# Kernel tuning notes

Hardware: AMD Instinct MI355X
Metric: run time of the kernel (lower is better)

The kernel has to match this reference:

```python
import jax, jax.numpy as jnp
import numpy as np
import math

B, N, NDIM = 8, 8192, 2
WIDTH, HEADS, OUT_C, LATENT_D = 128, 4, 128, 128
N_POINT, N_SAMPLE, RADIUS, PATCH = 128, 8, 0.2, 8
MAX_DEG = 15
POS_DIM = NDIM * (1 + 2 * MAX_DEG)  # 62
SELF_LAYERS = 3


def setup_inputs() -> dict:
    ks = jax.random.split(jax.random.key(0), 16)
    f32 = jnp.float32
    def nrm(k, shape, s=0.02):
        return jax.random.normal(k, shape, dtype=f32) * s
    W = WIDTH
    inp = {
        'points': jax.random.uniform(ks[0], (B, N, NDIM), dtype=f32),
        'pe_w': nrm(ks[1], (POS_DIM, W)), 'pe_b': jnp.zeros((W,), f32),
        'conv1_w': nrm(ks[2], (W, W + NDIM, PATCH, 1)), 'conv1_b': jnp.zeros((W,), f32),
        'conv2_w': nrm(ks[3], (W, W, PATCH, 1)), 'conv2_b': jnp.zeros((W,), f32),
        'output_tokens': jax.random.normal(ks[4], (LATENT_D, W), dtype=f32),
        'ln_pre_s': jnp.ones((W,), f32), 'ln_pre_b': jnp.zeros((W,), f32),
        'c_ln1_s': jnp.ones((W,), f32), 'c_ln1_b': jnp.zeros((W,), f32),
        'c_ln2_s': jnp.ones((W,), f32), 'c_ln2_b': jnp.zeros((W,), f32),
        'c_q_w': nrm(ks[5], (W, W)), 'c_q_b': jnp.zeros((W,), f32),
        'c_kv_w': nrm(ks[6], (W, 2 * W)), 'c_kv_b': jnp.zeros((2 * W,), f32),
        'c_proj_w': nrm(ks[7], (W, W)), 'c_proj_b': jnp.zeros((W,), f32),
        'c_ln3_s': jnp.ones((W,), f32), 'c_ln3_b': jnp.zeros((W,), f32),
        'c_mlp1_w': nrm(ks[8], (W, 4 * W)), 'c_mlp1_b': jnp.zeros((4 * W,), f32),
        'c_mlp2_w': nrm(ks[9], (4 * W, W)), 'c_mlp2_b': jnp.zeros((W,), f32),
        's_ln1_s': jnp.ones((SELF_LAYERS, W), f32), 's_ln1_b': jnp.zeros((SELF_LAYERS, W), f32),
        's_qkv_w': nrm(ks[10], (SELF_LAYERS, W, 3 * W)), 's_qkv_b': jnp.zeros((SELF_LAYERS, 3 * W), f32),
        's_proj_w': nrm(ks[11], (SELF_LAYERS, W, W)), 's_proj_b': jnp.zeros((SELF_LAYERS, W), f32),
        's_ln2_s': jnp.ones((SELF_LAYERS, W), f32), 's_ln2_b': jnp.zeros((SELF_LAYERS, W), f32),
        's_mlp1_w': nrm(ks[12], (SELF_LAYERS, W, 4 * W)), 's_mlp1_b': jnp.zeros((SELF_LAYERS, 4 * W), f32),
        's_mlp2_w': nrm(ks[13], (SELF_LAYERS, 4 * W, W)), 's_mlp2_b': jnp.zeros((SELF_LAYERS, W), f32),
        'ln_post_s': jnp.ones((W,), f32), 'ln_post_b': jnp.zeros((W,), f32),
        'out_w': nrm(ks[14], (W, OUT_C)), 'out_b': jnp.zeros((OUT_C,), f32),
    }
    return inp


def _layer_norm(x, s, b):
    m = jnp.mean(x, -1, keepdims=True)
    v = jnp.mean(jnp.square(x - m), -1, keepdims=True)
    return (x - m) * jax.lax.rsqrt(v + 1e-5) * s + b


def _posenc_nerf(x):
    # point-e nerf posenc: concat([x, sin(xb), sin(xb + pi/2)])
    scales = 2.0 ** jnp.arange(MAX_DEG, dtype=jnp.float32)
    xb = (x[..., None, :] * scales[:, None]).reshape(*x.shape[:-1], -1)
    emb = jnp.sin(jnp.concatenate([xb, xb + 0.5 * jnp.pi], axis=-1))
    return jnp.concatenate([x, emb], axis=-1)  # [..., C*(1+2*MAX_DEG)]


def _mha(q, k, v):
    b, tq, w = q.shape
    dh = w // HEADS
    qh = q.reshape(b, tq, HEADS, dh)
    kh = k.reshape(b, -1, HEADS, dh)
    vh = v.reshape(b, -1, HEADS, dh)
    scores = jnp.einsum('bqhd,bkhd->bhqk', qh, kh) * (1.0 / math.sqrt(dh))
    attn = jax.nn.softmax(scores, axis=-1)
    return jnp.einsum('bhqk,bkhd->bqhd', attn, vh).reshape(b, tq, w)


def _circ_conv(x, w, b):
    # Conv2d kernel (PATCH,1), stride 1, circular padding (PATCH//2, 0)
    p = PATCH // 2
    xp = jnp.concatenate([x[:, :, -p:], x, x[:, :, :p]], axis=2)
    y = jax.lax.conv_general_dilated(xp, w, (1, 1), 'VALID',
                                     dimension_numbers=('NCHW', 'OIHW', 'NCHW'))
    return y + b[None, :, None, None]


def _forward(points, pe_w, pe_b, conv1_w, conv1_b, conv2_w, conv2_b, output_tokens,
             ln_pre_s, ln_pre_b, c_ln1_s, c_ln1_b, c_ln2_s, c_ln2_b, c_q_w, c_q_b,
             c_kv_w, c_kv_b, c_proj_w, c_proj_b, c_ln3_s, c_ln3_b, c_mlp1_w, c_mlp1_b,
             c_mlp2_w, c_mlp2_b, s_ln1_s, s_ln1_b, s_qkv_w, s_qkv_b, s_proj_w, s_proj_b,
             s_ln2_s, s_ln2_b, s_mlp1_w, s_mlp1_b, s_mlp2_w, s_mlp2_b, ln_post_s, ln_post_b,
             out_w, out_b):
    bsz, n, _ = points.shape
    dataset_emb = _posenc_nerf(points) @ pe_w + pe_b             # [B,N,W]
    # ---- PointSetEmbedding (fps_method='first' -> first n_point centers) ----
    new_xyz = points[:, :N_POINT]                                # [B,S,2]
    sqr = jnp.sum(jnp.square(new_xyz[:, :, None] - points[:, None]), -1)  # [B,S,N]
    base = jnp.broadcast_to(jnp.arange(n, dtype=jnp.int32), sqr.shape)
    idx = jnp.where(sqr > RADIUS ** 2, n, base)
    idx = jnp.sort(idx, axis=-1)[:, :, :N_SAMPLE]
    idx = jnp.where(idx == n, idx[:, :, :1], idx)                # [B,S,K] ball-query indices
    gather = jax.vmap(lambda a, i: a[i])
    grouped_xyz = gather(points, idx) - new_xyz[:, :, None]      # [B,S,K,2] relative coords
    grouped_pts = gather(dataset_emb, idx)                       # [B,S,K,W]
    feats = jnp.concatenate([grouped_xyz, grouped_pts], -1)      # [B,S,K,W+2]
    x = jnp.transpose(feats, (0, 3, 2, 1))                       # [B,C,K,S]
    x = jax.nn.silu(_circ_conv(x, conv1_w, conv1_b))
    x = jax.nn.silu(_circ_conv(x, conv2_w, conv2_b))
    data_tokens = jnp.transpose(x.mean(axis=2), (0, 2, 1))       # [B,S,W]
    # ---- Perceiver: cross-attn then self-attn ----
    lat = jnp.broadcast_to(output_tokens[None], (bsz, LATENT_D, WIDTH))
    h = _layer_norm(jnp.concatenate([data_tokens, lat], axis=1), ln_pre_s, ln_pre_b)
    q = _layer_norm(h, c_ln1_s, c_ln1_b) @ c_q_w + c_q_b
    kv = _layer_norm(dataset_emb, c_ln2_s, c_ln2_b) @ c_kv_w + c_kv_b
    k, v = jnp.split(kv, 2, axis=-1)
    h = h + (_mha(q, k, v) @ c_proj_w + c_proj_b)
    t = _layer_norm(h, c_ln3_s, c_ln3_b)
    h = h + (jax.nn.gelu(t @ c_mlp1_w + c_mlp1_b, approximate=False) @ c_mlp2_w + c_mlp2_b)
    for i in range(SELF_LAYERS):
        qkv = _layer_norm(h, s_ln1_s[i], s_ln1_b[i]) @ s_qkv_w[i] + s_qkv_b[i]
        q, k, v = jnp.split(qkv, 3, axis=-1)
        h = h + (_mha(q, k, v) @ s_proj_w[i] + s_proj_b[i])
        t = _layer_norm(h, s_ln2_s[i], s_ln2_b[i])
        h = h + (jax.nn.gelu(t @ s_mlp1_w[i] + s_mlp1_b[i], approximate=False) @ s_mlp2_w[i] + s_mlp2_b[i])
    h = h[:, -LATENT_D:]
    return jnp.tanh(_layer_norm(h, ln_post_s, ln_post_b) @ out_w + out_b)


def reference(points, pe_w, pe_b, conv1_w, conv1_b, conv2_w, conv2_b, output_tokens,
              ln_pre_s, ln_pre_b, c_ln1_s, c_ln1_b, c_ln2_s, c_ln2_b, c_q_w, c_q_b,
              c_kv_w, c_kv_b, c_proj_w, c_proj_b, c_ln3_s, c_ln3_b, c_mlp1_w, c_mlp1_b,
              c_mlp2_w, c_mlp2_b, s_ln1_s, s_ln1_b, s_qkv_w, s_qkv_b, s_proj_w, s_proj_b,
              s_ln2_s, s_ln2_b, s_mlp1_w, s_mlp1_b, s_mlp2_w, s_mlp2_b, ln_post_s, ln_post_b,
              out_w, out_b):
    return _forward(points, pe_w, pe_b, conv1_w, conv1_b, conv2_w, conv2_b, output_tokens,
                    ln_pre_s, ln_pre_b, c_ln1_s, c_ln1_b, c_ln2_s, c_ln2_b, c_q_w, c_q_b,
                    c_kv_w, c_kv_b, c_proj_w, c_proj_b, c_ln3_s, c_ln3_b, c_mlp1_w, c_mlp1_b,
                    c_mlp2_w, c_mlp2_b, s_ln1_s, s_ln1_b, s_qkv_w, s_qkv_b, s_proj_w, s_proj_b,
                    s_ln2_s, s_ln2_b, s_mlp1_w, s_mlp1_b, s_mlp2_w, s_mlp2_b, ln_post_s, ln_post_b,
                    out_w, out_b)
```

## Files before the change

kernel.cpp:

```cpp
#include <hip/hip_runtime.h>
#include <math.h>


namespace {

constexpr int NP = 8192;
constexpr int WD = 128;
constexpr int POSD = 62;
constexpr float R2C = 0.04f;
constexpr float QSCALE = 0.17677669529663687f;
constexpr float HALFPI = 1.5707963705062866f;

typedef __bf16 bf16x8 __attribute__((ext_vector_type(8)));
typedef float f32x4 __attribute__((ext_vector_type(4)));
union U16B { uint4 u; bf16x8 h; unsigned short s[8]; };

__device__ __forceinline__ float b2f(unsigned short u) {
  unsigned v = (unsigned)u << 16;
  return __builtin_bit_cast(float, v);
}

constexpr size_t AO_WQ     = 0;
constexpr size_t AO_WKV    = 16384;
constexpr size_t AO_WPROJC = 49152;
constexpr size_t AO_WMLP1C = 65536;
constexpr size_t AO_WMLP2C = 131072;
constexpr size_t AO_WQKVS  = 196608;
constexpr size_t AO_WPROJS = 344064;
constexpr size_t AO_WMLP1S = 393216;
constexpr size_t AO_WMLP2S = 589824;
constexpr size_t AO_WOUT   = 786432;
constexpr size_t AO_W1B    = 802816;
constexpr size_t AO_W2B    = 937984;
constexpr size_t AO_TOT    = 1069056;

__global__ __launch_bounds__(256) void k_posenc(
    const float* __restrict__ pts, const float* __restrict__ pew,
    const float* __restrict__ peb, unsigned short* __restrict__ embb) {
  __shared__ float posT[62][36];
  const int tid = threadIdx.x;
  const int base = blockIdx.x * 32;
  for (int i = tid; i < 32 * POSD; i += 256) {
    int p = i / POSD, j = i % POSD;
    const float* pp = pts + (size_t)(base + p) * 2;
    float v;
    if (j < 2) {
      v = pp[j];
    } else if (j < 32) {
      int t = j - 2;
      v = sinf(pp[t & 1] * (float)(1 << (t >> 1)));
    } else {
      int t = j - 32;
      v = sinf(pp[t & 1] * (float)(1 << (t >> 1)) + HALFPI);
    }
    posT[j][p] = v;
  }
  __syncthreads();
  const int c = tid & 127, pg = tid >> 7;
  float acc[16];
  const float bias = peb[c];
#pragma unroll
  for (int k = 0; k < 16; ++k) acc[k] = bias;
  for (int j = 0; j < POSD; ++j) {
    float w = pew[j * WD + c];
    const float4 p0 = *(const float4*)&posT[j][pg * 16];
    const float4 p1 = *(const float4*)&posT[j][pg * 16 + 4];
    const float4 p2 = *(const float4*)&posT[j][pg * 16 + 8];
    const float4 p3 = *(const float4*)&posT[j][pg * 16 + 12];
    acc[0] += p0.x * w;  acc[1] += p0.y * w;
    acc[2] += p0.z * w;  acc[3] += p0.w * w;
    acc[4] += p1.x * w;  acc[5] += p1.y * w;
    acc[6] += p1.z * w;  acc[7] += p1.w * w;
    acc[8] += p2.x * w;  acc[9] += p2.y * w;
    acc[10] += p2.z * w; acc[11] += p2.w * w;
    acc[12] += p3.x * w; acc[13] += p3.y * w;
    acc[14] += p3.z * w; acc[15] += p3.w * w;
  }
#pragma unroll
  for (int k = 0; k < 16; ++k) {
    __bf16 bv = (__bf16)acc[k];
    embb[(size_t)(base + pg * 16 + k) * WD + c] = *(unsigned short*)&bv;
  }
}

__global__ __launch_bounds__(256) void k_prep(
    const float* __restrict__ wq, const float* __restrict__ wkv,
    const float* __restrict__ wprojc, const float* __restrict__ wmlp1c,
    const float* __restrict__ wmlp2c, const float* __restrict__ wqkvs,
    const float* __restrict__ wprojs, const float* __restrict__ wmlp1s,
    const float* __restrict__ wmlp2s, const float* __restrict__ wout,
    const float* __restrict__ w1, const float* __restrict__ w2,
    unsigned short* __restrict__ dst) {
  const size_t i = (size_t)blockIdx.x * 256 + threadIdx.x;
  if (i >= AO_TOT) return;
  float v;
  if (i < AO_WKV) {
    size_t j = i;            v = wq[(j & 127) * 128 + (j >> 7)];
  } else if (i < AO_WPROJC) {
    size_t j = i - AO_WKV;   v = wkv[(j & 127) * 256 + (j >> 7)];
  } else if (i < AO_WMLP1C) {
    size_t j = i - AO_WPROJC; v = wprojc[(j & 127) * 128 + (j >> 7)];
  } else if (i < AO_WMLP2C) {
    size_t j = i - AO_WMLP1C; v = wmlp1c[(j & 127) * 512 + (j >> 7)];
  } else if (i < AO_WQKVS) {
    size_t j = i - AO_WMLP2C; v = wmlp2c[(j & 511) * 128 + (j >> 9)];
  } else if (i < AO_WPROJS) {
    size_t j = i - AO_WQKVS;
    size_t L = j / 49152, jj = j % 49152;
    v = wqkvs[L * 49152 + (jj & 127) * 384 + (jj >> 7)];
  } else if (i < AO_WMLP1S) {
    size_t j = i - AO_WPROJS;
    size_t L = j / 16384, jj = j % 16384;
    v = wprojs[L * 16384 + (jj & 127) * 128 + (jj >> 7)];
  } else if (i < AO_WMLP2S) {
    size_t j = i - AO_WMLP1S;
    size_t L = j / 65536, jj = j % 65536;
    v = wmlp1s[L * 65536 + (jj & 127) * 512 + (jj >> 7)];
  } else if (i < AO_WOUT) {
    size_t j = i - AO_WMLP2S;
    size_t L = j / 65536, jj = j % 65536;
    v = wmlp2s[L * 65536 + (jj & 511) * 128 + (jj >> 9)];
  } else if (i < AO_W1B) {
    size_t j = i - AO_WOUT;  v = wout[(j & 127) * 128 + (j >> 7)];
  } else if (i < AO_W2B) {
    size_t j = i - AO_W1B;
    size_t c = j / 1056, k = j % 1056;
    v = (k < 1040) ? w1[c * 1040 + k] : 0.f;
  } else {
    size_t j = i - AO_W2B;   v = w2[(j >> 10) * 1024 + (j & 1023)];
  }
  __bf16 bv = (__bf16)v;
  dst[i] = *(unsigned short*)&bv;
}

__global__ __launch_bounds__(256) void k_kvgc(
    const unsigned short* __restrict__ embb,
    const unsigned short* __restrict__ wkvt,
    const float* __restrict__ kvbias, unsigned short* __restrict__ kb,
    unsigned short* __restrict__ vb, const float* __restrict__ lnS,
    const float* __restrict__ lnB, const float* __restrict__ pts,
    const unsigned short* __restrict__ w1b, const float* __restrict__ b1,
    const unsigned short* __restrict__ w2b, const float* __restrict__ b2,
    float* __restrict__ dtok) {
  __shared__ __align__(16) char shl[43776];
  __shared__ int sid[4][8];
  const int bx = blockIdx.x;
  const int tid = threadIdx.x;
  const int w = tid >> 6, lane = tid & 63;
  const int l15 = lane & 15, l16 = lane >> 4;

  if (bx >= 256) {
    const int kx = bx - 256;
    const size_t row0 = (size_t)kx * 32;
    unsigned short (*Ab)[136] = (unsigned short(*)[136])shl;
    unsigned short (*Bt)[136] = (unsigned short(*)[136])(shl + 8704);
    {
      const int n = tid >> 1, hf = tid & 1;
      const unsigned short* src = wkvt + ((size_t)n * 128 + hf * 64);
#pragma unroll
      for (int q8 = 0; q8 < 8; ++q8)
        *(uint4*)&Bt[n][hf * 64 + q8 * 8] = *(const uint4*)(src + q8 * 8);
    }
    {
      const int r = tid >> 3, seg = tid & 7;
      const unsigned short* ap = embb + (row0 + r) * WD + seg * 16;
      U16B w0, w1u;
      w0.u = *(const uint4*)ap;
      w1u.u = *(const uint4*)(ap + 8);
      float xv[16];
#pragma unroll
      for (int j = 0; j < 8; ++j) {
        xv[j] = b2f(w0.s[j]);
        xv[8 + j] = b2f(w1u.s[j]);
      }
      float s = 0.f, sq = 0.f;
#pragma unroll
      for (int j = 0; j < 16; ++j) { s += xv[j]; sq += xv[j] * xv[j]; }
      s += __shfl_xor(s, 1);  sq += __shfl_xor(sq, 1);
      s += __shfl_xor(s, 2);  sq += __shfl_xor(sq, 2);
      s += __shfl_xor(s, 4);  sq += __shfl_xor(sq, 4);
      const float m = s * (1.f / 128.f);
      const float var = fmaxf(sq * (1.f / 128.f) - m * m, 0.f);
      const float rinv = 1.0f / sqrtf(var + 1e-5f);
      U16B u0, u1;
#pragma unroll
      for (int j = 0; j < 16; ++j) {
        int col = seg * 16 + j;
        float y = (xv[j] - m) * rinv * lnS[col] + lnB[col];
        if (j < 8) u0.h[j] = (__bf16)y; else u1.h[j - 8] = (__bf16)y;
      }
      *(uint4*)&Ab[r][seg * 16] = u0.u;
      *(uint4*)&Ab[r][seg * 16 + 8] = u1.u;
    }
    const int rt = w >> 1, ch = w & 1;
    for (int nb = 0; nb < 2; ++nb) {
      if (nb) {
        __syncthreads();
        const int n = tid >> 1, hf = tid & 1;
        const unsigned short* src =
            wkvt + ((size_t)(128 + n) * 128 + hf * 64);
#pragma unroll
        for (int q8 = 0; q8 < 8; ++q8)
          *(uint4*)&Bt[n][hf * 64 + q8 * 8] = *(const uint4*)(src + q8 * 8);
      }
      __syncthreads();
      f32x4 acc[4];
#pragma unroll
      for (int j = 0; j < 4; ++j) acc[j] = (f32x4){0.f, 0.f, 0.f, 0.f};
#pragma unroll
      for (int kk = 0; kk < 4; ++kk) {
        U16B ua;
        ua.u = *(const uint4*)&Ab[rt * 16 + l15][kk * 32 + l16 * 8];
#pragma unroll
        for (int ct4 = 0; ct4 < 4; ++ct4) {
          U16B ub;
          ub.u =
              *(const uint4*)&Bt[(ch * 4 + ct4) * 16 + l15][kk * 32 + l16 * 8];
          acc[ct4] = __builtin_amdgcn_mfma_f32_16x16x32_bf16(ua.h, ub.h,
                                                             acc[ct4], 0, 0, 0);
        }
      }
      unsigned short* Dp = nb ? vb : kb;
#pragma unroll
      for (int ct4 = 0; ct4 < 4; ++ct4) {
        int colL = (ch * 4 + ct4) * 16 + l15;
        float bv = kvbias[nb * 128 + colL];
#pragma unroll
        for (int r = 0; r < 4; ++r) {
          size_t row = row0 + rt * 16 + l16 * 4 + r;
          __bf16 ov = (__bf16)(acc[ct4][r] + bv);
          Dp[row * 128 + colL] = *(unsigned short*)&ov;
        }
      }
    }
    return;
  }

  const int b = bx >> 5;
  const int i0 = (bx & 31) * 4;
  unsigned short* ftp  = (unsigned short*)shl;
  unsigned short* Bt1p = (unsigned short*)(shl + 8448);
  unsigned short* y1p  = (unsigned short*)shl;
  unsigned short* Bt2p = (unsigned short*)(shl + 16384);
  float* tmpp = (float*)(shl + 16384);

  {
    const int i = i0 + w;
    const float cx = pts[((size_t)b * NP + i) * 2];
    const float cy = pts[((size_t)b * NP + i) * 2 + 1];
    int cnt = 0;
    for (int j0 = 0; j0 < NP; j0 += 64) {
      int j = j0 + lane;
      float dx = pts[((size_t)b * NP + j) * 2] - cx;
      float dy = pts[((size_t)b * NP + j) * 2 + 1] - cy;
      float d2 = __fadd_rn(__fmul_rn(dx, dx), __fmul_rn(dy, dy));
      bool ok = !(d2 > R2C);
      unsigned long long m = __ballot(ok);
      int ord = cnt + __popcll(m & ((1ull << lane) - 1ull));
      if (ok && ord < 8) sid[w][ord] = j;
      cnt += (int)__popcll(m);
      if (cnt >= 8) break;
    }
    if (lane < 8 && lane >= cnt) sid[w][lane] = sid[w][0];
  }
  __syncthreads();
  {
    const int pr = tid >> 3, c16 = tid & 7;
    const int pt = pr >> 3, s = pr & 7;
    const unsigned short* src =
        embb + ((size_t)b * NP + sid[pt][s]) * WD + c16 * 16;
    U16B u0, u1;
    u0.u = *(const uint4*)src;
    u1.u = *(const uint4*)(src + 8);
#pragma unroll
    for (int j = 0; j < 8; ++j) {
      ftp[((size_t)pt * 132 + 2 + c16 * 16 + j) * 8 + s] = u0.s[j];
      ftp[((size_t)pt * 132 + 2 + c16 * 16 + 8 + j) * 8 + s] = u1.s[j];
    }
  }
  if (tid < 64) {
    int pt = tid >> 4, rem = tid & 15;
    int s = rem >> 1, d = rem & 1;
    float dv = pts[((size_t)b * NP + sid[pt][s]) * 2 + d] -
               pts[((size_t)b * NP + i0 + pt) * 2 + d];
    __bf16 bv = (__bf16)dv;
    ftp[((size_t)pt * 132 + d) * 8 + s] = *(unsigned short*)&bv;
    int pt2 = tid >> 4, cin2 = 130 + ((tid >> 3) & 1), s2 = tid & 7;
    ftp[((size_t)pt2 * 132 + cin2) * 8 + s2] = 0;
  }
  __syncthreads();
  f32x4 acc1[2][2];
#pragma unroll
  for (int t = 0; t < 2; ++t)
#pragma unroll
    for (int bt = 0; bt < 2; ++bt) acc1[t][bt] = (f32x4){0.f, 0.f, 0.f, 0.f};
  for (int ps = 0; ps < 2; ++ps) {
    const int cinbase = ps ? 68 : 0;
    const int CW = ps ? 64 : 68;
    if (ps) __syncthreads();
    {
      const int n = tid >> 3, g = tid & 7;
      const int pt = n >> 3, h = n & 7;
#pragma unroll
      for (int it = 0; it < 9; ++it) {
        int cl = g + it * 8;
        if (cl < CW) {
          int cin = cinbase + cl;
          U16B u0, u;
          u0.u = *(const uint4*)&ftp[((size_t)pt * 132 + cin) * 8];
#pragma unroll
          for (int p = 0; p < 8; ++p) u.s[p] = u0.s[(h + p + 4) & 7];
          *(uint4*)&Bt1p[n * 552 + cl * 8] = u.u;
        }
      }
    }
    __syncthreads();
    const unsigned short* w1r =
        w1b + (size_t)(w * 32 + l15) * 1056 + cinbase * 8;
    const int kit = ps ? 16 : 17;
    for (int ks = 0; ks < kit; ++ks) {
      const int k0 = ks * 32 + l16 * 8;
      U16B a0, a1, b0, b1u;
      a0.u = *(const uint4*)(w1r + k0);
      a1.u = *(const uint4*)(w1r + 16 * 1056 + k0);
      b0.u = *(const uint4*)&Bt1p[l15 * 552 + k0];
      b1u.u = *(const uint4*)&Bt1p[(16 + l15) * 552 + k0];
      acc1[0][0] = __builtin_amdgcn_mfma_f32_16x16x32_bf16(a0.h, b0.h,
                                                           acc1[0][0], 0, 0, 0);
      acc1[0][1] = __builtin_amdgcn_mfma_f32_16x16x32_bf16(a0.h, b1u.h,
                                                           acc1[0][1], 0, 0, 0);
      acc1[1][0] = __builtin_amdgcn_mfma_f32_16x16x32_bf16(a1.h, b0.h,
                                                           acc1[1][0], 0, 0, 0);
      acc1[1][1] = __builtin_amdgcn_mfma_f32_16x16x32_bf16(a1.h, b1u.h,
                                                           acc1[1][1], 0, 0, 0);
    }
  }
  __syncthreads();
  {
#pragma unroll
    for (int t = 0; t < 2; ++t)
#pragma unroll
      for (int bt = 0; bt < 2; ++bt) {
        const int n = bt * 16 + l15;
        const int pt = n >> 3, h = n & 7;
#pragma unroll
        for (int r = 0; r < 4; ++r) {
          int c = w * 32 + t * 16 + l16 * 4 + r;
          float x = acc1[t][bt][r] + b1[c];
          float sy = x / (1.f + __expf(-x));
          __bf16 bh = (__bf16)sy;
          unsigned short bits = *(unsigned short*)&bh;
          size_t yb = ((size_t)pt * 128 + c) * 16;
          y1p[yb + h] = bits;
          if (h == 0) y1p[yb + 8] = bits;
        }
      }
  }
  f32x4 acc2[2][3];
#pragma unroll
  for (int t = 0; t < 2; ++t)
#pragma unroll
    for (int bt = 0; bt < 3; ++bt) acc2[t][bt] = (f32x4){0.f, 0.f, 0.f, 0.f};
  for (int ps = 0; ps < 4; ++ps) {
    __syncthreads();
    {
      const int g = tid & 7;
      for (int n2 = tid >> 3; n2 < 38; n2 += 32) {
        const int pt = n2 / 9, h2 = n2 % 9;
#pragma unroll
        for (int it = 0; it < 4; ++it) {
          int cl = g + it * 8;
          U16B o;
          if (n2 < 36) {
            int c1 = ps * 32 + cl;
            size_t yb = ((size_t)pt * 128 + c1) * 16;
            U16B u0;
            u0.u = *(const uint4*)&y1p[yb];
            unsigned short yv[9];
#pragma unroll
            for (int j = 0; j < 8; ++j) yv[j] = u0.s[j];
            yv[8] = y1p[yb + 8];
#pragma unroll
            for (int p = 0; p < 8; ++p) o.s[p] = yv[(h2 + p + 5) % 9];
          } else {
            o.u.x = o.u.y = o.u.z = o.u.w = 0;
          }
          *(uint4*)&Bt2p[n2 * 264 + cl * 8] = o.u;
        }
      }
    }
    __syncthreads();
    const unsigned short* w2r =
        w2b + (size_t)(w * 32 + l15) * 1024 + ps * 256;
    int r2 = 32 + l15;
    if (r2 > 37) r2 = 37;
#pragma unroll
    for (int ks = 0; ks < 8; ++ks) {
      const int k0 = ks * 32 + l16 * 8;
      U16B a0, a1, b0, b1u, b2u;
      a0.u = *(const uint4*)(w2r + k0);
      a1.u = *(const uint4*)(w2r + 16 * 1024 + k0);
      b0.u = *(const uint4*)&Bt2p[l15 * 264 + k0];
      b1u.u = *(const uint4*)&Bt2p[(16 + l15) * 264 + k0];
      b2u.u = *(const uint4*)&Bt2p[r2 * 264 + k0];
      acc2[0][0] = __builtin_amdgcn_mfma_f32_16x16x32_bf16(a0.h, b0.h,
                                                           acc2[0][0], 0, 0, 0);
      acc2[0][1] = __builtin_amdgcn_mfma_f32_16x16x32_bf16(a0.h, b1u.h,
                                                           acc2[0][1], 0, 0, 0);
      acc2[0][2] = __builtin_amdgcn_mfma_f32_16x16x32_bf16(a0.h, b2u.h,
                                                           acc2[0][2], 0, 0, 0);
      acc2[1][0] = __builtin_amdgcn_mfma_f32_16x16x32_bf16(a1.h, b0.h,
                                                           acc2[1][0], 0, 0, 0);
      acc2[1][1] = __builtin_amdgcn_mfma_f32_16x16x32_bf16(a1.h, b1u.h,
                                                           acc2[1][1], 0, 0, 0);
      acc2[1][2] = __builtin_amdgcn_mfma_f32_16x16x32_bf16(a1.h, b2u.h,
                                                           acc2[1][2], 0, 0, 0);
    }
  }
  __syncthreads();
  {
#pragma unroll
    for (int t = 0; t < 2; ++t)
#pragma unroll
      for (int bt = 0; bt < 3; ++bt) {
        const int n2 = bt * 16 + l15;
        if (n2 < 36) {
          const int h2 = n2 % 9;
          const float wgt = (h2 == 0) ? 2.f : 1.f;
#pragma unroll
          for (int r = 0; r < 4; ++r) {
            int c = w * 32 + t * 16 + l16 * 4 + r;
            float x = acc2[t][bt][r] + b2[c];
            tmpp[n2 * 132 + c] = wgt * (x / (1.f + __expf(-x)));
          }
        }
      }
  }
  __syncthreads();
#pragma unroll
  for (int k = 0; k < 2; ++k) {
    int idx = tid + k * 256;
    int pt = idx >> 7, c = idx & 127;
    float ssum = 0.f;
#pragma unroll
    for (int h2 = 0; h2 < 9; ++h2) ssum += tmpp[(pt * 9 + h2) * 132 + c];
    dtok[((size_t)b * 128 + i0 + pt) * WD + c] = ssum / 10.0f;
  }
}

__global__ __launch_bounds__(64) void k_concat_ln(
    const float* __restrict__ dtok, const float* __restrict__ otok,
    const float* __restrict__ g, const float* __restrict__ bta,
    float* __restrict__ h0) {
  const int row = blockIdx.x;
  const int b = row >> 8, t = row & 255;
  const int lane = threadIdx.x;
  const float* src = (t < 128) ? (dtok + ((size_t)b * 128 + t) * WD)
                               : (otok + (size_t)(t - 128) * WD);
  const float2 x2 = *(const float2*)(src + lane * 2);
  float s = x2.x + x2.y;
  float sq = x2.x * x2.x + x2.y * x2.y;
#pragma unroll
  for (int o = 1; o < 64; o <<= 1) {
    s += __shfl_xor(s, o);
    sq += __shfl_xor(sq, o);
  }
  float m = s * (1.f / 128.f);
  float var = fmaxf(sq * (1.f / 128.f) - m * m, 0.f);
  float r = 1.0f / sqrtf(var + 1e-5f);
  int c = lane * 2;
  float2 o2;
  o2.x = (x2.x - m) * r * g[c] + bta[c];
  o2.y = (x2.y - m) * r * g[c + 1] + bta[c + 1];
  *(float2*)(h0 + (size_t)row * WD + c) = o2;
}

template <int ABF, int OBF, int COMB>
__global__ __launch_bounds__(256) void k_bgemm16(
    const void* __restrict__ A, int lda, const unsigned short* __restrict__ wt,
    const float* __restrict__ bias, const float* __restrict__ res, int ldres,
    void* __restrict__ D, int ldd, int K, int act,
    const float* __restrict__ lnS, const float* __restrict__ lnB, int keep,
    int skip, float oscale, int scaleCols,
    const unsigned short* __restrict__ opart, const float* __restrict__ lbuf,
    int S) {
  __shared__ unsigned short Ab[16][136];
  __shared__ unsigned short Bt[64][136];
  const int tid = threadIdx.x;
  const int row0 = blockIdx.x * 16;
  const int col0 = blockIdx.y * 64;
  const int w = tid >> 6, lane = tid & 63;
  const int l15 = lane & 15, l16 = lane >> 4;
  f32x4 acc = (f32x4){0.f, 0.f, 0.f, 0.f};
  for (int kt = 0; kt < K; kt += 128) {
    if (kt) __syncthreads();
    {
      const int n = tid >> 2, q = tid & 3;
      const unsigned short* src = wt + (size_t)(col0 + n) * K + kt + q * 32;
      *(uint4*)&Bt[n][q * 32] = *(const uint4*)src;
      *(uint4*)&Bt[n][q * 32 + 8] = *(const uint4*)(src + 8);
      *(uint4*)&Bt[n][q * 32 + 16] = *(const uint4*)(src + 16);
      *(uint4*)&Bt[n][q * 32 + 24] = *(const uint4*)(src + 24);
    }
    {
      const int r = tid >> 4, seg = tid & 15;
      const int grow = row0 + r;
      if (COMB) {
        const int bq = grow >> 8, q = grow & 255;
        const int h = seg >> 2, d0 = (seg & 3) * 8;
        const int pb = (bq * 4 + h) * S;
        float L = 0.f;
        float vals[8] = {0.f, 0.f, 0.f, 0.f, 0.f, 0.f, 0.f, 0.f};
        for (int s = 0; s < S; ++s) {
          L += lbuf[(size_t)(pb + s) * 256 + q];
          uint4 p4 = *(const uint4*)(opart + (size_t)(pb + s) * 8192 + q * 32 + d0);
          const unsigned short* ps = (const unsigned short*)&p4;
#pragma unroll
          for (int j = 0; j < 8; ++j) vals[j] += b2f(ps[j]);
        }
        const float inv = 1.0f / L;
        U16B u0;
#pragma unroll
        for (int j = 0; j < 8; ++j) u0.h[j] = (__bf16)(vals[j] * inv);
        *(uint4*)&Ab[r][seg * 8] = u0.u;
      } else if (ABF) {
        const int srow = (grow / keep) * (keep + skip) + skip + grow % keep;
        const unsigned short* ap =
            (const unsigned short*)A + (size_t)srow * lda + kt + seg * 8;
        *(uint4*)&Ab[r][seg * 8] = *(const uint4*)ap;
      } else {
        const int srow = (grow / keep) * (keep + skip) + skip + grow % keep;
        const float* ap = (const float*)A + (size_t)srow * lda + kt + seg * 8;
        float4 v0 = *(const float4*)ap;
        float4 v1 = *(const float4*)(ap + 4);
        float xv[8] = {v0.x, v0.y, v0.z, v0.w, v1.x, v1.y, v1.z, v1.w};
        if (lnS != nullptr) {
          float s = 0.f, sq = 0.f;
#pragma unroll
          for (int j = 0; j < 8; ++j) { s += xv[j]; sq += xv[j] * xv[j]; }
          s += __shfl_xor(s, 1);  sq += __shfl_xor(sq, 1);
          s += __shfl_xor(s, 2);  sq += __shfl_xor(sq, 2);
          s += __shfl_xor(s, 4);  sq += __shfl_xor(sq, 4);
          s += __shfl_xor(s, 8);  sq += __shfl_xor(sq, 8);
          const float m = s * (1.f / 128.f);
          const float var = fmaxf(sq * (1.f / 128.f) - m * m, 0.f);
          const float rinv = 1.0f / sqrtf(var + 1e-5f);
#pragma unroll
          for (int j = 0; j < 8; ++j) {
            int col = seg * 8 + j;
            xv[j] = (xv[j] - m) * rinv * lnS[col] + lnB[col];
          }
        }
        U16B u0;
#pragma unroll
        for (int j = 0; j < 8; ++j) u0.h[j] = (__bf16)xv[j];
        *(uint4*)&Ab[r][seg * 8] = u0.u;
      }
    }
    __syncthreads();
#pragma unroll
    for (int kk = 0; kk < 4; ++kk) {
      U16B ua, ub;
      ua.u = *(const uint4*)&Ab[l15][kk * 32 + l16 * 8];
      ub.u = *(const uint4*)&Bt[w * 16 + l15][kk * 32 + l16 * 8];
      acc = __builtin_amdgcn_mfma_f32_16x16x32_bf16(ua.h, ub.h, acc, 0, 0, 0);
    }
  }
  {
    const int colL = w * 16 + l15;
    const int col = col0 + colL;
    const float bv = bias[col];
#pragma unroll
    for (int r = 0; r < 4; ++r) {
      const int row = row0 + l16 * 4 + r;
      float x = acc[r] + bv;
      if (col0 < scaleCols) x *= oscale;
      if (act == 1) x = 0.5f * x * (1.0f + erff(x * 0.7071067811865476f));
      else if (act == 2) x = tanhf(x);
      if (res != nullptr) x += res[(size_t)row * ldres + col];
      if (OBF) {
        __bf16 ov = (__bf16)x;
        ((unsigned short*)D)[(size_t)row * ldd + col] = *(unsigned short*)&ov;
      } else {
        ((float*)D)[(size_t)row * ldd + col] = x;
      }
    }
  }
}

__global__ __launch_bounds__(256) void k_attn_mfma(
    const unsigned short* __restrict__ Q, int qs,
    const unsigned short* __restrict__ K, int ks,
    const unsigned short* __restrict__ V, int vs,
    unsigned short* __restrict__ opart, float* __restrict__ lbuf, int Tk,
    int S, int CH) {
  const int bx = blockIdx.x;
  const int s = bx % S;
  const int bh = bx / S;
  const int h = bh & 3, b = bh >> 2;
  const int tid = threadIdx.x;
  const int w = tid >> 6, lane = tid & 63;
  const int l15 = lane & 15, l16 = lane >> 4;

  __shared__ unsigned short Vt[32 * 68];
  __shared__ unsigned short Pl[4][16 * 72];

  bf16x8 qf[4];
#pragma unroll
  for (int m = 0; m < 4; ++m) {
    U16B u;
    u.u = *(const uint4*)(Q + (size_t)(b * 256 + w * 64 + m * 16 + l15) * qs +
                          h * 32 + l16 * 8);
    qf[m] = u.h;
  }
  U16B uones;
#pragma unroll
  for (int j = 0; j < 8; ++j) uones.h[j] = (__bf16)1.0f;
  const bf16x8 ones = uones.h;

  f32x4 o[4][2];
#pragma unroll
  for (int m = 0; m < 4; ++m)
#pragma unroll
    for (int d = 0; d < 2; ++d) o[m][d] = (f32x4){0.f, 0.f, 0.f, 0.f};
  f32x4 lsum[4];
#pragma unroll
  for (int m = 0; m < 4; ++m) lsum[m] = (f32x4){0.f, 0.f, 0.f, 0.f};

  const int kt0 = s * CH;
  for (int kt = kt0; kt < kt0 + CH; kt += 64) {
    __syncthreads();
    {
      const int r = tid >> 2, c0 = (tid & 3) * 8;
      const unsigned short* vp =
          V + (size_t)(b * Tk + kt + r) * vs + h * 32 + c0;
      U16B uv;
      uv.u = *(const uint4*)vp;
#pragma unroll
      for (int j = 0; j < 8; ++j) Vt[(c0 + j) * 68 + r] = uv.s[j];
    }
    __syncthreads();

    bf16x8 kf[4];
#pragma unroll
    for (int ksb = 0; ksb < 4; ++ksb) {
      U16B u;
      u.u = *(const uint4*)(K + (size_t)(b * Tk + kt + ksb * 16 + l15) * ks +
                            h * 32 + l16 * 8);
      kf[ksb] = u.h;
    }
    bf16x8 vf[2][2];
#pragma unroll
    for (int kc = 0; kc < 2; ++kc)
#pragma unroll
      for (int d = 0; d < 2; ++d) {
        const unsigned short* vp =
            &Vt[(l15 + 16 * d) * 68 + kc * 32 + l16 * 8];
        U16B u;
        *(uint2*)&u.s[0] = *(const uint2*)vp;
        *(uint2*)&u.s[4] = *(const uint2*)(vp + 4);
        vf[kc][d] = u.h;
      }

#pragma unroll
    for (int m = 0; m < 4; ++m) {
      const f32x4 zf = {0.f, 0.f, 0.f, 0.f};
      f32x4 sf[4];
#pragma unroll
      for (int ksb = 0; ksb < 4; ++ksb)
        sf[ksb] = __builtin_amdgcn_mfma_f32_16x16x32_bf16(qf[m], kf[ksb], zf,
                                                          0, 0, 0);
#pragma unroll
      for (int ksb = 0; ksb < 4; ++ksb)
#pragma unroll
        for (int r = 0; r < 4; ++r) {
          float p = __expf(sf[ksb][r]);
          __bf16 pb = (__bf16)p;
          Pl[w][(l16 * 4 + r) * 72 + ksb * 16 + l15] = *(unsigned short*)&pb;
        }
      asm volatile("s_waitcnt lgkmcnt(0)" ::: "memory");
      bf16x8 pa[2];
#pragma unroll
      for (int kc = 0; kc < 2; ++kc) {
        U16B u;
        u.u = *(const uint4*)&Pl[w][l15 * 72 + kc * 32 + l16 * 8];
        pa[kc] = u.h;
      }
      lsum[m] = __builtin_amdgcn_mfma_f32_16x16x32_bf16(pa[0], ones, lsum[m],
                                                        0, 0, 0);
      lsum[m] = __builtin_amdgcn_mfma_f32_16x16x32_bf16(pa[1], ones, lsum[m],
                                                        0, 0, 0);
#pragma unroll
      for (int kc = 0; kc < 2; ++kc)
#pragma unroll
        for (int d = 0; d < 2; ++d)
          o[m][d] = __builtin_amdgcn_mfma_f32_16x16x32_bf16(pa[kc], vf[kc][d],
                                                            o[m][d], 0, 0, 0);
    }
  }

  const size_t ob = (size_t)bx * 8192;
#pragma unroll
  for (int m = 0; m < 4; ++m) {
    int qrow = w * 64 + m * 16 + l16 * 4;
#pragma unroll
    for (int r = 0; r < 4; ++r) {
#pragma unroll
      for (int d = 0; d < 2; ++d) {
        __bf16 bo = (__bf16)o[m][d][r];
        opart[ob + (qrow + r) * 32 + d * 16 + l15] = *(unsigned short*)&bo;
      }
      if (l15 == 0) lbuf[(size_t)bx * 256 + qrow + r] = lsum[m][r];
    }
  }
}

}

extern "C" void kernel_launch(void* const* d_in, const int* in_sizes, int n_in,
                              void* d_out, int out_size, void* d_ws,
                              size_t ws_size, hipStream_t stream) {
  const float* pts      = (const float*)d_in[0];
  const float* pe_w     = (const float*)d_in[1];
  const float* pe_b     = (const float*)d_in[2];
  const float* conv1_w  = (const float*)d_in[3];
  const float* conv1_b  = (const float*)d_in[4];
  const float* conv2_w  = (const float*)d_in[5];
  const float* conv2_b  = (const float*)d_in[6];
  const float* otok     = (const float*)d_in[7];
  const float* ln_pre_s = (const float*)d_in[8];
  const float* ln_pre_b = (const float*)d_in[9];
  const float* c_ln1_s  = (const float*)d_in[10];
  const float* c_ln1_b  = (const float*)d_in[11];
  const float* c_ln2_s  = (const float*)d_in[12];
  const float* c_ln2_b  = (const float*)d_in[13];
  const float* c_q_w    = (const float*)d_in[14];
  const float* c_q_b    = (const float*)d_in[15];
  const float* c_kv_w   = (const float*)d_in[16];
  const float* c_kv_b   = (const float*)d_in[17];
  const float* c_proj_w = (const float*)d_in[18];
  const float* c_proj_b = (const float*)d_in[19];
  const float* c_ln3_s  = (const float*)d_in[20];
  const float* c_ln3_b  = (const float*)d_in[21];
  const float* c_mlp1_w = (const float*)d_in[22];
  const float* c_mlp1_b = (const float*)d_in[23];
  const float* c_mlp2_w = (const float*)d_in[24];
  const float* c_mlp2_b = (const float*)d_in[25];
  const float* s_ln1_s  = (const float*)d_in[26];
  const float* s_ln1_b  = (const float*)d_in[27];
  const float* s_qkv_w  = (const float*)d_in[28];
  const float* s_qkv_b  = (const float*)d_in[29];
  const float* s_proj_w = (const float*)d_in[30];
  const float* s_proj_b = (const float*)d_in[31];
  const float* s_ln2_s  = (const float*)d_in[32];
  const float* s_ln2_b  = (const float*)d_in[33];
  const float* s_mlp1_w = (const float*)d_in[34];
  const float* s_mlp1_b = (const float*)d_in[35];
  const float* s_mlp2_w = (const float*)d_in[36];
  const float* s_mlp2_b = (const float*)d_in[37];
  const float* lnpost_s = (const float*)d_in[38];
  const float* lnpost_b = (const float*)d_in[39];
  const float* out_w    = (const float*)d_in[40];
  const float* out_b    = (const float*)d_in[41];

  char* ws = (char*)d_ws;
  constexpr size_t MB = 1024 * 1024;
  unsigned short* embb = (unsigned short*)(ws);
  unsigned short* kbuf = (unsigned short*)(ws + 32 * MB);
  unsigned short* vbuf = (unsigned short*)(ws + 48 * MB);
  char*  b3   = ws + 64 * MB;
  float* dtok = (float*)(b3);
  float* hbuf = (float*)(b3 + 524288);
  unsigned short* qbuf = (unsigned short*)(b3 + 524288 + 1048576);
  unsigned short* mid = (unsigned short*)(b3 + 524288 + 3145728);
  unsigned short* qkv = (unsigned short*)(b3 + 524288 + 7340032);
  unsigned short* arena = (unsigned short*)(b3 + 524288 + 10485760);
  unsigned short* opart = (unsigned short*)(ws);
  float* lbuf  = (float*)(b3 + 16 * MB);

  const int IDK = 1 << 28;

  k_prep<<<(int)((AO_TOT + 255) / 256), 256, 0, stream>>>(
      c_q_w, c_kv_w, c_proj_w, c_mlp1_w, c_mlp2_w, s_qkv_w, s_proj_w,
      s_mlp1_w, s_mlp2_w, out_w, conv1_w, conv2_w, arena);
  k_posenc<<<2048, 256, 0, stream>>>(pts, pe_w, pe_b, embb);
  k_kvgc<<<2304, 256, 0, stream>>>(embb, arena + AO_WKV, c_kv_b, kbuf, vbuf,
                                   c_ln2_s, c_ln2_b, pts, arena + AO_W1B,
                                   conv1_b, arena + AO_W2B, conv2_b, dtok);
  k_concat_ln<<<2048, 64, 0, stream>>>(dtok, otok, ln_pre_s, ln_pre_b, hbuf);
  k_bgemm16<0, 1, 0><<<dim3(128, 2), 256, 0, stream>>>(
      hbuf, 128, arena + AO_WQ, c_q_b, nullptr, 0, qbuf, 128, 128, 0, c_ln1_s,
      c_ln1_b, IDK, 0, QSCALE, 128, nullptr, nullptr, 0);
  k_attn_mfma<<<1024, 256, 0, stream>>>(qbuf, 128, kbuf, 128, vbuf, 128,
                                        opart, lbuf, 8192, 32, 256);
  k_bgemm16<0, 0, 1><<<dim3(128, 2), 256, 0, stream>>>(
      nullptr, 128, arena + AO_WPROJC, c_proj_b, hbuf, 128, hbuf, 128, 128, 0,
      nullptr, nullptr, IDK, 0, 1.f, 0, opart, lbuf, 32);
  k_bgemm16<0, 1, 0><<<dim3(128, 8), 256, 0, stream>>>(
      hbuf, 128, arena + AO_WMLP1C, c_mlp1_b, nullptr, 0, mid, 512, 128, 1,
      c_ln3_s, c_ln3_b, IDK, 0, 1.f, 0, nullptr, nullptr, 0);
  k_bgemm16<1, 0, 0><<<dim3(128, 2), 256, 0, stream>>>(
      mid, 512, arena + AO_WMLP2C, c_mlp2_b, hbuf, 128, hbuf, 128, 512, 0,
      nullptr, nullptr, IDK, 0, 1.f, 0, nullptr, nullptr, 0);
  for (int i = 0; i < 3; ++i) {
    k_bgemm16<0, 1, 0><<<dim3(128, 6), 256, 0, stream>>>(
        hbuf, 128, arena + AO_WQKVS + (size_t)i * 49152, s_qkv_b + i * 384,
        nullptr, 0, qkv, 384, 128, 0, s_ln1_s + i * 128, s_ln1_b + i * 128,
        IDK, 0, QSCALE, 128, nullptr, nullptr, 0);
    k_attn_mfma<<<128, 256, 0, stream>>>(qkv, 384, qkv + 128, 384, qkv + 256,
                                         384, opart, lbuf, 256, 4, 64);
    k_bgemm16<0, 0, 1><<<dim3(128, 2), 256, 0, stream>>>(
        nullptr, 128, arena + AO_WPROJS + (size_t)i * 16384,
        s_proj_b + i * 128, hbuf, 128, hbuf, 128, 128, 0, nullptr, nullptr,
        IDK, 0, 1.f, 0, opart, lbuf, 4);
    k_bgemm16<0, 1, 0><<<dim3(128, 8), 256, 0, stream>>>(
        hbuf, 128, arena + AO_WMLP1S + (size_t)i * 65536, s_mlp1_b + i * 512,
        nullptr, 0, mid, 512, 128, 1, s_ln2_s + i * 128, s_ln2_b + i * 128,
        IDK, 0, 1.f, 0, nullptr, nullptr, 0);
    k_bgemm16<1, 0, 0><<<dim3(128, 2), 256, 0, stream>>>(
        mid, 512, arena + AO_WMLP2S + (size_t)i * 65536, s_mlp2_b + i * 128,
        hbuf, 128, hbuf, 128, 512, 0, nullptr, nullptr, IDK, 0, 1.f, 0,
        nullptr, nullptr, 0);
  }
  k_bgemm16<0, 0, 0><<<dim3(64, 2), 256, 0, stream>>>(
      hbuf, 128, arena + AO_WOUT, out_b, nullptr, 0, (float*)d_out, 128, 128,
      2, lnpost_s, lnpost_b, 128, 128, 1.f, 0, nullptr, nullptr, 0);
}
```

Before: 231.6 us.

## Fuse attention combine, projection, LayerNorm and MLP into one post-attention kernel

Adds a k_post kernel that merges the split-attention partials, applies the output projection with residual, LayerNorm, MLP1 with GELU and MLP2 with residual, all for a 16-row tile kept in shared memory. It replaces three bgemm launches per transformer block (four blocks in total) and drops the mid buffer round-trip through global memory. The trade-off is that each fused kernel runs only 128 blocks instead of 256 to 1024, and every block streams all the weights itself, so parallelism drops and weight reads repeat across blocks. It also adds a no-op index expression to one dtok store.

New measurement: 246.4 us. 1.06x slower.

```diff
diff --git a/kernel.cpp b/kernel.cpp
--- a/kernel.cpp
+++ b/kernel.cpp
@@ -444,7 +444,8 @@
     float ssum = 0.f;
 #pragma unroll
     for (int h2 = 0; h2 < 9; ++h2) ssum += tmpp[(pt * 9 + h2) * 132 + c];
-    dtok[((size_t)b * 128 + i0 + pt) * WD + c] = ssum / 10.0f;
+    dtok[((size_t)b * NP / 64 + 0) * 0 + ((size_t)b * 128 + i0 + pt) * WD + c] =
+        ssum / 10.0f;
   }
 }
 
@@ -475,15 +476,13 @@
   *(float2*)(h0 + (size_t)row * WD + c) = o2;
 }
 
-template <int ABF, int OBF, int COMB>
+template <int ABF, int OBF>
 __global__ __launch_bounds__(256) void k_bgemm16(
     const void* __restrict__ A, int lda, const unsigned short* __restrict__ wt,
     const float* __restrict__ bias, const float* __restrict__ res, int ldres,
     void* __restrict__ D, int ldd, int K, int act,
     const float* __restrict__ lnS, const float* __restrict__ lnB, int keep,
-    int skip, float oscale, int scaleCols,
-    const unsigned short* __restrict__ opart, const float* __restrict__ lbuf,
-    int S) {
+    int skip, float oscale, int scaleCols) {
   __shared__ unsigned short Ab[16][136];
   __shared__ unsigned short Bt[64][136];
   const int tid = threadIdx.x;
@@ -505,31 +504,12 @@
     {
       const int r = tid >> 4, seg = tid & 15;
       const int grow = row0 + r;
-      if (COMB) {
-        const int bq = grow >> 8, q = grow & 255;
-        const int h = seg >> 2, d0 = (seg & 3) * 8;
-        const int pb = (bq * 4 + h) * S;
-        float L = 0.f;
-        float vals[8] = {0.f, 0.f, 0.f, 0.f, 0.f, 0.f, 0.f, 0.f};
-        for (int s = 0; s < S; ++s) {
-          L += lbuf[(size_t)(pb + s) * 256 + q];
-          uint4 p4 = *(const uint4*)(opart + (size_t)(pb + s) * 8192 + q * 32 + d0);
-          const unsigned short* ps = (const unsigned short*)&p4;
-#pragma unroll
-          for (int j = 0; j < 8; ++j) vals[j] += b2f(ps[j]);
-        }
-        const float inv = 1.0f / L;
-        U16B u0;
-#pragma unroll
-        for (int j = 0; j < 8; ++j) u0.h[j] = (__bf16)(vals[j] * inv);
-        *(uint4*)&Ab[r][seg * 8] = u0.u;
-      } else if (ABF) {
-        const int srow = (grow / keep) * (keep + skip) + skip + grow % keep;
+      const int srow = (grow / keep) * (keep + skip) + skip + grow % keep;
+      if (ABF) {
         const unsigned short* ap =
             (const unsigned short*)A + (size_t)srow * lda + kt + seg * 8;
         *(uint4*)&Ab[r][seg * 8] = *(const uint4*)ap;
       } else {
-        const int srow = (grow / keep) * (keep + skip) + skip + grow % keep;
         const float* ap = (const float*)A + (size_t)srow * lda + kt + seg * 8;
         float4 v0 = *(const float4*)ap;
         float4 v1 = *(const float4*)(ap + 4);
@@ -584,6 +564,171 @@
       } else {
         ((float*)D)[(size_t)row * ldd + col] = x;
       }
+    }
+  }
+}
+
+__global__ __launch_bounds__(256) void k_post(
+    const unsigned short* __restrict__ opart, const float* __restrict__ lbuf,
+    int S, const unsigned short* __restrict__ wproj,
+    const float* __restrict__ bproj, const unsigned short* __restrict__ w1,
+    const float* __restrict__ b1m, const unsigned short* __restrict__ w2,
+    const float* __restrict__ b2m, const float* __restrict__ lnS,
+    const float* __restrict__ lnB, float* __restrict__ hbuf) {
+  __shared__ unsigned short Att[16][136];
+  __shared__ unsigned short Bt[64][136];
+  __shared__ unsigned short LNr[16][136];
+  __shared__ unsigned short Mt[16][520];
+  __shared__ float Hrow[16][132];
+  const int tid = threadIdx.x;
+  const int row0 = blockIdx.x * 16;
+  const int w = tid >> 6, lane = tid & 63;
+  const int l15 = lane & 15, l16 = lane >> 4;
+
+  {
+    const int r = tid >> 4, seg = tid & 15;
+    const int grow = row0 + r;
+    const int bq = grow >> 8, q = grow & 255;
+    const int h = seg >> 2, d0 = (seg & 3) * 8;
+    const int pb = (bq * 4 + h) * S;
+    float L = 0.f;
+    float vals[8] = {0.f, 0.f, 0.f, 0.f, 0.f, 0.f, 0.f, 0.f};
+    for (int s = 0; s < S; ++s) {
+      L += lbuf[(size_t)(pb + s) * 256 + q];
+      uint4 p4 = *(const uint4*)(opart + (size_t)(pb + s) * 8192 + q * 32 + d0);
+      const unsigned short* ps = (const unsigned short*)&p4;
+#pragma unroll
+      for (int j = 0; j < 8; ++j) vals[j] += b2f(ps[j]);
+    }
+    const float inv = 1.0f / L;
+    U16B u0;
+#pragma unroll
+    for (int j = 0; j < 8; ++j) u0.h[j] = (__bf16)(vals[j] * inv);
+    *(uint4*)&Att[r][seg * 8] = u0.u;
+  }
+  f32x4 accp[2];
+  for (int cp = 0; cp < 2; ++cp) {
+    if (cp) __syncthreads();
+    {
+      const int n = tid >> 2, q = tid & 3;
+      const unsigned short* src = wproj + (size_t)(cp * 64 + n) * 128 + q * 32;
+      *(uint4*)&Bt[n][q * 32] = *(const uint4*)src;
+      *(uint4*)&Bt[n][q * 32 + 8] = *(const uint4*)(src + 8);
+      *(uint4*)&Bt[n][q * 32 + 16] = *(const uint4*)(src + 16);
+      *(uint4*)&Bt[n][q * 32 + 24] = *(const uint4*)(src + 24);
+    }
+    __syncthreads();
+    accp[cp] = (f32x4){0.f, 0.f, 0.f, 0.f};
+#pragma unroll
+    for (int kk = 0; kk < 4; ++kk) {
+      U16B ua, ub;
+      ua.u = *(const uint4*)&Att[l15][kk * 32 + l16 * 8];
+      ub.u = *(const uint4*)&Bt[w * 16 + l15][kk * 32 + l16 * 8];
+      accp[cp] =
+          __builtin_amdgcn_mfma_f32_16x16x32_bf16(ua.h, ub.h, accp[cp], 0, 0, 0);
+    }
+  }
+  __syncthreads();
+#pragma unroll
+  for (int cp = 0; cp < 2; ++cp) {
+    const int col = cp * 64 + w * 16 + l15;
+    const float bv = bproj[col];
+#pragma unroll
+    for (int r = 0; r < 4; ++r) {
+      const int rloc = l16 * 4 + r;
+      float x = accp[cp][r] + bv + hbuf[(size_t)(row0 + rloc) * WD + col];
+      Hrow[rloc][col] = x;
+    }
+  }
+  __syncthreads();
+  {
+    const int r = tid >> 4, seg = tid & 15;
+    float xv[8];
+#pragma unroll
+    for (int j = 0; j < 8; ++j) xv[j] = Hrow[r][seg * 8 + j];
+    float s = 0.f, sq = 0.f;
+#pragma unroll
+    for (int j = 0; j < 8; ++j) { s += xv[j]; sq += xv[j] * xv[j]; }
+    s += __shfl_xor(s, 1);  sq += __shfl_xor(sq, 1);
+    s += __shfl_xor(s, 2);  sq += __shfl_xor(sq, 2);
+    s += __shfl_xor(s, 4);  sq += __shfl_xor(sq, 4);
+    s += __shfl_xor(s, 8);  sq += __shfl_xor(sq, 8);
+    const float m = s * (1.f / 128.f);
+    const float var = fmaxf(sq * (1.f / 128.f) - m * m, 0.f);
+    const float rinv = 1.0f / sqrtf(var + 1e-5f);
+    U16B u0;
+#pragma unroll
+    for (int j = 0; j < 8; ++j) {
+      int col = seg * 8 + j;
+      u0.h[j] = (__bf16)((xv[j] - m) * rinv * lnS[col] + lnB[col]);
+    }
+    *(uint4*)&LNr[r][seg * 8] = u0.u;
+  }
+  __syncthreads();
+  for (int nc = 0; nc < 8; ++nc) {
+    {
+      const int n = tid >> 2, q = tid & 3;
+      const unsigned short* src = w1 + (size_t)(nc * 64 + n) * 128 + q * 32;
+      *(uint4*)&Bt[n][q * 32] = *(const uint4*)src;
+      *(uint4*)&Bt[n][q * 32 + 8] = *(const uint4*)(src + 8);
+      *(uint4*)&Bt[n][q * 32 + 16] = *(const uint4*)(src + 16);
+      *(uint4*)&Bt[n][q * 32 + 24] = *(const uint4*)(src + 24);
+    }
+    __syncthreads();
+    f32x4 acc = (f32x4){0.f, 0.f, 0.f, 0.f};
+#pragma unroll
+    for (int kk = 0; kk < 4; ++kk) {
+      U16B ua, ub;
+      ua.u = *(const uint4*)&LNr[l15][kk * 32 + l16 * 8];
+      ub.u = *(const uint4*)&Bt[w * 16 + l15][kk * 32 + l16 * 8];
+      acc = __builtin_amdgcn_mfma_f32_16x16x32_bf16(ua.h, ub.h, acc, 0, 0, 0);
+    }
+    const int colL = w * 16 + l15;
+    const float bv = b1m[nc * 64 + colL];
+#pragma unroll
+    for (int r = 0; r < 4; ++r) {
+      float x = acc[r] + bv;
+      x = 0.5f * x * (1.0f + erff(x * 0.7071067811865476f));
+      __bf16 ov = (__bf16)x;
+      Mt[l16 * 4 + r][nc * 64 + colL] = *(unsigned short*)&ov;
+    }
+    __syncthreads();
+  }
+  f32x4 acc2[2];
+  acc2[0] = (f32x4){0.f, 0.f, 0.f, 0.f};
+  acc2[1] = (f32x4){0.f, 0.f, 0.f, 0.f};
+  for (int cp = 0; cp < 2; ++cp) {
+    for (int kt = 0; kt < 4; ++kt) {
+      {
+        const int n = tid >> 2, q = tid & 3;
+        const unsigned short* src =
+            w2 + (size_t)(cp * 64 + n) * 512 + kt * 128 + q * 32;
+        *(uint4*)&Bt[n][q * 32] = *(const uint4*)src;
+        *(uint4*)&Bt[n][q * 32 + 8] = *(const uint4*)(src + 8);
+        *(uint4*)&Bt[n][q * 32 + 16] = *(const uint4*)(src + 16);
+        *(uint4*)&Bt[n][q * 32 + 24] = *(const uint4*)(src + 24);
+      }
+      __syncthreads();
+#pragma unroll
+      for (int kk = 0; kk < 4; ++kk) {
+        U16B ua, ub;
+        ua.u = *(const uint4*)&Mt[l15][kt * 128 + kk * 32 + l16 * 8];
+        ub.u = *(const uint4*)&Bt[w * 16 + l15][kk * 32 + l16 * 8];
+        acc2[cp] =
+            __builtin_amdgcn_mfma_f32_16x16x32_bf16(ua.h, ub.h, acc2[cp], 0, 0, 0);
+      }
+      __syncthreads();
+    }
+  }
+#pragma unroll
+  for (int cp = 0; cp < 2; ++cp) {
+    const int col = cp * 64 + w * 16 + l15;
+    const float bv = b2m[col];
+#pragma unroll
+    for (int r = 0; r < 4; ++r) {
+      const int rloc = l16 * 4 + r;
+      hbuf[(size_t)(row0 + rloc) * WD + col] =
+          acc2[cp][r] + bv + Hrow[rloc][col];
     }
   }
 }
@@ -772,7 +917,6 @@
   float* dtok = (float*)(b3);
   float* hbuf = (float*)(b3 + 524288);
   unsigned short* qbuf = (unsigned short*)(b3 + 524288 + 1048576);
-  unsigned short* mid = (unsigned short*)(b3 + 524288 + 3145728);
   unsigned short* qkv = (unsigned short*)(b3 + 524288 + 7340032);
   unsigned short* arena = (unsigned short*)(b3 + 524288 + 10485760);
   unsigned short* opart = (unsigned short*)(ws);
@@ -788,41 +932,29 @@
                                    c_ln2_s, c_ln2_b, pts, arena + AO_W1B,
                                    conv1_b, arena + AO_W2B, conv2_b, dtok);
   k_concat_ln<<<2048, 64, 0, stream>>>(dtok, otok, ln_pre_s, ln_pre_b, hbuf);
-  k_bgemm16<0, 1, 0><<<dim3(128, 2), 256, 0, stream>>>(
+  k_bgemm16<0, 1><<<dim3(128, 2), 256, 0, stream>>>(
       hbuf, 128, arena + AO_WQ, c_q_b, nullptr, 0, qbuf, 128, 128, 0, c_ln1_s,
-      c_ln1_b, IDK, 0, QSCALE, 128, nullptr, nullptr, 0);
+      c_ln1_b, IDK, 0, QSCALE, 128);
   k_attn_mfma<<<1024, 256, 0, stream>>>(qbuf, 128, kbuf, 128, vbuf, 128,
                                         opart, lbuf, 8192, 32, 256);
-  k_bgemm16<0, 0, 1><<<dim3(128, 2), 256, 0, stream>>>(
-      nullptr, 128, arena + AO_WPROJC, c_proj_b, hbuf, 128, hbuf, 128, 128, 0,
-      nullptr, nullptr, IDK, 0, 1.f, 0, opart, lbuf, 32);
-  k_bgemm16<0, 1, 0><<<dim3(128, 8), 256, 0, stream>>>(
-      hbuf, 128, arena + AO_WMLP1C, c_mlp1_b, nullptr, 0, mid, 512, 128, 1,
-      c_ln3_s, c_ln3_b, IDK, 0, 1.f, 0, nullptr, nullptr, 0);
-  k_bgemm16<1, 0, 0><<<dim3(128, 2), 256, 0, stream>>>(
-      mid, 512, arena + AO_WMLP2C, c_mlp2_b, hbuf, 128, hbuf, 128, 512, 0,
-      nullptr, nullptr, IDK, 0, 1.f, 0, nullptr, nullptr, 0);
+  k_post<<<128, 256, 0, stream>>>(opart, lbuf, 32, arena + AO_WPROJC,
+                                  c_proj_b, arena + AO_WMLP1C, c_mlp1_b,
+                                  arena + AO_WMLP2C, c_mlp2_b, c_ln3_s,
+                                  c_ln3_b, hbuf);
   for (int i = 0; i < 3; ++i) {
-    k_bgemm16<0, 1, 0><<<dim3(128, 6), 256, 0, stream>>>(
+    k_bgemm16<0, 1><<<dim3(128, 6), 256, 0, stream>>>(
         hbuf, 128, arena + AO_WQKVS + (size_t)i * 49152, s_qkv_b + i * 384,
         nullptr, 0, qkv, 384, 128, 0, s_ln1_s + i * 128, s_ln1_b + i * 128,
-        IDK, 0, QSCALE, 128, nullptr, nullptr, 0);
+        IDK, 0, QSCALE, 128);
     k_attn_mfma<<<128, 256, 0, stream>>>(qkv, 384, qkv + 128, 384, qkv + 256,
                                          384, opart, lbuf, 256, 4, 64);
-    k_bgemm16<0, 0, 1><<<dim3(128, 2), 256, 0, stream>>>(
-        nullptr, 128, arena + AO_WPROJS + (size_t)i * 16384,
-        s_proj_b + i * 128, hbuf, 128, hbuf, 128, 128, 0, nullptr, nullptr,
-        IDK, 0, 1.f, 0, opart, lbuf, 4);
-    k_bgemm16<0, 1, 0><<<dim3(128, 8), 256, 0, stream>>>(
-        hbuf, 128, arena + AO_WMLP1S + (size_t)i * 65536, s_mlp1_b + i * 512,
-        nullptr, 0, mid, 512, 128, 1, s_ln2_s + i * 128, s_ln2_b + i * 128,
-        IDK, 0, 1.f, 0, nullptr, nullptr, 0);
-    k_bgemm16<1, 0, 0><<<dim3(128, 2), 256, 0, stream>>>(
-        mid, 512, arena + AO_WMLP2S + (size_t)i * 65536, s_mlp2_b + i * 128,
-        hbuf, 128, hbuf, 128, 512, 0, nullptr, nullptr, IDK, 0, 1.f, 0,
-        nullptr, nullptr, 0);
-  }
-  k_bgemm16<0, 0, 0><<<dim3(64, 2), 256, 0, stream>>>(
+    k_post<<<128, 256, 0, stream>>>(
+        opart, lbuf, 4, arena + AO_WPROJS + (size_t)i * 16384,
+        s_proj_b + i * 128, arena + AO_WMLP1S + (size_t)i * 65536,
+        s_mlp1_b + i * 512, arena + AO_WMLP2S + (size_t)i * 65536,
+        s_mlp2_b + i * 128, s_ln2_s + i * 128, s_ln2_b + i * 128, hbuf);
+  }
+  k_bgemm16<0, 0><<<dim3(64, 2), 256, 0, stream>>>(
       hbuf, 128, arena + AO_WOUT, out_b, nullptr, 0, (float*)d_out, 128, 128,
-      2, lnpost_s, lnpost_b, 128, 128, 1.f, 0, nullptr, nullptr, 0);
+      2, lnpost_s, lnpost_b, 128, 128, 1.f, 0);
 }
```
